# Performance work log

Measured on AMD Instinct MI355X. Metric: run time of the kernel, lower is better.

## Reference

```python
import jax, jax.numpy as jnp
import numpy as np

NUM_CLASSES = 1000
NUM_NEIGHBOURS = 200
SIGMA = 10.0
GAUSS_CONST = 1.0 / (2.0 * SIGMA ** 2)


def setup_inputs() -> dict:
    key = jax.random.key(0)
    k1, k2, k3 = jax.random.split(key, 3)
    B, D, C = 512, 512, 100000
    features = jax.random.normal(k1, (B, D), dtype=jnp.float32)
    centres = jax.random.normal(k2, (C, D), dtype=jnp.float32)
    centre_labels = jax.random.randint(k3, (C,), 0, NUM_CLASSES)
    weight = jnp.zeros((C,), dtype=jnp.float32)
    return {"features": features, "centres": centres,
            "centre_labels": centre_labels, "weight": weight}


def _knn(features, centres, k):
    # squared euclidean distances [B, C] without materializing [B, C, D]
    f2 = jnp.sum(features * features, axis=1, keepdims=True)      # [B,1]
    c2 = jnp.sum(centres * centres, axis=1)                        # [C]
    d2 = f2 + c2[None, :] - 2.0 * features @ centres.T             # [B,C]
    _, idx = jax.lax.top_k(-d2, k)                                 # smallest k
    return idx                                                     # [B,k]


def reference(features, centres, centre_labels, weight):
    B = features.shape[0]
    K = NUM_NEIGHBOURS
    nbr = _knn(features, centres, K)                               # [B,K] int
    gathered = centres[nbr]                                        # [B,K,D]
    d2 = jnp.sum((features[:, None, :] - gathered) ** 2, axis=-1)  # [B,K]
    kernel_weights = jnp.exp(weight)                               # [C]
    d = jnp.exp(-d2 * GAUSS_CONST) * kernel_weights[nbr]           # [B,K]
    nbr_labels = centre_labels[nbr]                                # [B,K]
    rows = jnp.arange(B)[:, None]
    p = jnp.zeros((B, NUM_CLASSES), dtype=d.dtype).at[rows, nbr_labels].add(d)
    p = jnp.where(p == 0, 1e-10, p)
    p = p / jnp.sum(p, axis=1, keepdims=True)
    return jnp.log(p)
```

## Files before the change

### kernel.cpp

```cpp
#include <hip/hip_runtime.h>
#include <hip/hip_fp16.h>
#include <math.h>
#include <stdint.h>

#define D_DIM    512
#define NCLS     1000
#define KSEL     200
#define NBINS    1024
#define HREP     4
#define CAND_MAX 2048
#define GCONST   0.005
#define MARGIN   4.0f

typedef short s8v __attribute__((ext_vector_type(8)));
typedef float f4v __attribute__((ext_vector_type(4)));

#define GLOAD_LDS16(gp, lp) __builtin_amdgcn_global_load_lds( \
    (const __attribute__((address_space(1))) void*)(gp),      \
    (__attribute__((address_space(3))) void*)(lp), 16, 0, 0)

static __device__ __forceinline__ unsigned short f2bf(float x) {
    unsigned u = __float_as_uint(x);
    return (unsigned short)((u + 0x7FFFu + ((u >> 16) & 1u)) >> 16);
}

static __device__ __forceinline__ unsigned cvt_pk_bf16(float lo, float hi) {
    unsigned r;
    asm("v_cvt_pk_bf16_f32 %0, %1, %2" : "=v"(r) : "v"(lo), "v"(hi));
    return r;
}

__global__ __launch_bounds__(256)
void convertF(const float* __restrict__ F, unsigned short* __restrict__ Fb,
              float* __restrict__ f2)
{
    __shared__ float red[256];
    const int r = blockIdx.x, t = threadIdx.x;
    float2 v = *(const float2*)(F + (size_t)r * D_DIM + t * 2);
    ushort2 o; o.x = f2bf(v.x); o.y = f2bf(v.y);
    *(ushort2*)(Fb + (size_t)r * D_DIM + t * 2) = o;
    red[t] = v.x * v.x + v.y * v.y;
    __syncthreads();
    for (int off = 128; off > 0; off >>= 1) {
        if (t < off) red[t] += red[t + off];
        __syncthreads();
    }
    if (t == 0) f2[r] = red[0];
}

__global__ __launch_bounds__(512)
void mfma_gemm(const unsigned short* __restrict__ Fb,
               const float* __restrict__ C,
               const float* __restrict__ f2,
               __half* __restrict__ Dm, int N)
{
    __shared__ short smem[2 * 256 * 64 + 128 * 64];
    short* BsBase = smem + 2 * 256 * 64;
    const int t    = threadIdx.x;
    const int lane = t & 63;
    const int w    = t >> 6;
    const int wm   = w >> 1, wn = w & 1;
    const int m0   = blockIdx.x * 256;
    const int n0   = blockIdx.y * 128;
    const int lrow = lane >> 3;
    const int oct  = (lane & 7) ^ lrow;
    const int quad = lane >> 4;
    const int col  = lane & 15;

    f4v acc[4][4];
#pragma unroll
    for (int i = 0; i < 4; ++i)
#pragma unroll
        for (int j = 0; j < 4; ++j) acc[i][j] = (f4v){0.f, 0.f, 0.f, 0.f};

    float  c2part[2] = {0.f, 0.f};
    float4 ra[2], rb[2];

#pragma unroll
    for (int cc = 0; cc < 2; ++cc) {
        int row = (w * 2 + cc) * 8 + lrow;
        int rg  = n0 + row; rg = rg < N ? rg : N - 1;
        const float* gp = C + (size_t)rg * D_DIM + oct * 8;
        ra[cc] = *(const float4*)gp;
        rb[cc] = *(const float4*)(gp + 4);
    }
#pragma unroll
    for (int cc = 0; cc < 4; ++cc) {
        int ch = w * 4 + cc;
        GLOAD_LDS16(Fb + (size_t)(m0 + ch * 8 + lrow) * D_DIM + 0 + oct * 8,
                    &smem[ch * 512]);
    }

    int buf = 0;
    for (int k0 = 0; k0 < D_DIM; k0 += 64, buf ^= 1) {
        short* As  = smem + buf * (256 * 64);
        short* Asn = smem + (buf ^ 1) * (256 * 64);
        short* Bs  = BsBase;

#pragma unroll
        for (int cc = 0; cc < 2; ++cc) {
            int row = (w * 2 + cc) * 8 + lrow;
            float4 va = ra[cc], vb = rb[cc];
            c2part[cc] += va.x*va.x + va.y*va.y + va.z*va.z + va.w*va.w
                        + vb.x*vb.x + vb.y*vb.y + vb.z*vb.z + vb.w*vb.w;
            uint4 o;
            o.x = cvt_pk_bf16(va.x, va.y);
            o.y = cvt_pk_bf16(va.z, va.w);
            o.z = cvt_pk_bf16(vb.x, vb.y);
            o.w = cvt_pk_bf16(vb.z, vb.w);
            *(uint4*)&Bs[row * 64 + (lane & 7) * 8] = o;
        }

        if (k0 + 64 < D_DIM) {
#pragma unroll
            for (int cc = 0; cc < 2; ++cc) {
                int row = (w * 2 + cc) * 8 + lrow;
                int rg  = n0 + row; rg = rg < N ? rg : N - 1;
                const float* gp = C + (size_t)rg * D_DIM + (k0 + 64) + oct * 8;
                ra[cc] = *(const float4*)gp;
                rb[cc] = *(const float4*)(gp + 4);
            }
#pragma unroll
            for (int cc = 0; cc < 4; ++cc) {
                int ch = w * 4 + cc;
                GLOAD_LDS16(Fb + (size_t)(m0 + ch * 8 + lrow) * D_DIM
                                + (k0 + 64) + oct * 8,
                            &Asn[ch * 512]);
            }
            asm volatile("s_waitcnt vmcnt(8) lgkmcnt(0)" ::: "memory");
        } else {
            asm volatile("s_waitcnt vmcnt(0) lgkmcnt(0)" ::: "memory");
        }
        __builtin_amdgcn_s_barrier();
        asm volatile("" ::: "memory");

#pragma unroll
        for (int kk = 0; kk < 2; ++kk) {
            int slot = (kk * 4 + quad) ^ (col & 7);
            s8v b[4];
#pragma unroll
            for (int j = 0; j < 4; ++j) {
                int row = wn * 64 + j * 16 + col;
                b[j] = *(s8v*)&Bs[row * 64 + slot * 8];
            }
            s8v a[4];
#pragma unroll
            for (int i = 0; i < 4; ++i) {
                int row = wm * 64 + i * 16 + col;
                a[i] = *(s8v*)&As[row * 64 + slot * 8];
            }
#pragma unroll
            for (int i = 0; i < 4; ++i)
#pragma unroll
                for (int j = 0; j < 4; ++j)
                    acc[i][j] = __builtin_amdgcn_mfma_f32_16x16x32_bf16(
                        a[i], b[j], acc[i][j], 0, 0, 0);
        }
        __builtin_amdgcn_s_barrier();
        asm volatile("" ::: "memory");
    }

    float* c2s = (float*)BsBase;
#pragma unroll
    for (int cc = 0; cc < 2; ++cc) {
        float s = c2part[cc];
        s += __shfl_xor(s, 1, 64);
        s += __shfl_xor(s, 2, 64);
        s += __shfl_xor(s, 4, 64);
        int row = (w * 2 + cc) * 8 + lrow;
        if ((lane & 7) == 0) c2s[row] = s;
    }
    __syncthreads();

    float c2v[4];
#pragma unroll
    for (int j = 0; j < 4; ++j)
        c2v[j] = c2s[wn * 64 + j * 16 + col];
    float fv[4][4];
#pragma unroll
    for (int i = 0; i < 4; ++i)
#pragma unroll
        for (int v = 0; v < 4; ++v)
            fv[i][v] = f2[m0 + wm * 64 + i * 16 + quad * 4 + v];

    __half* Cs = (__half*)smem;
#pragma unroll
    for (int h = 0; h < 2; ++h) {
        __syncthreads();
        if ((wm >> 1) == h) {
            int mlb = (wm & 1) * 64;
#pragma unroll
            for (int i = 0; i < 4; ++i) {
#pragma unroll
                for (int j = 0; j < 4; ++j) {
#pragma unroll
                    for (int v = 0; v < 4; ++v) {
                        int ml = mlb + i * 16 + quad * 4 + v;
                        int nl = wn * 64 + j * 16 + col;
                        float d2 = fv[i][v] + c2v[j] - 2.f * acc[i][j][v];
                        int slot = (nl >> 3) ^ (ml & 7);
                        Cs[ml * 128 + slot * 8 + (nl & 7)] = __float2half(d2);
                    }
                }
            }
        }
        __syncthreads();
#pragma unroll
        for (int it = 0; it < 4; ++it) {
            int idx = it * 512 + t;
            int row = idx >> 4;
            int o8  = idx & 15;
            int n   = n0 + o8 * 8;
            const __half* src = &Cs[row * 128 + ((o8 ^ (row & 7)) * 8)];
            __half* dst = Dm + (size_t)(m0 + h * 128 + row) * N + n;
            if (n + 7 < N) {
                *(uint4*)dst = *(const uint4*)src;
            } else if (n < N) {
                for (int e = 0; e < 8 && n + e < N; ++e) dst[e] = src[e];
            }
        }
    }
}

__global__ __launch_bounds__(1024)
void fused_select(const __half* __restrict__ Dm,
                  const float* __restrict__ F, const float* __restrict__ C,
                  const int* __restrict__ labels, const float* __restrict__ weight,
                  float* __restrict__ out, int N)
{
    __shared__ unsigned hist[NBINS * HREP];
    __shared__ float    fs[D_DIM];
    __shared__ int      idxs[CAND_MAX];
    __shared__ double   dists[CAND_MAX];
    __shared__ float    p[NCLS];
    __shared__ float    red[1024];
    __shared__ unsigned scanbuf[256];
    __shared__ float    sT;
    __shared__ unsigned scnt;

    const int r = blockIdx.x, t = threadIdx.x;
    for (int b = t; b < NBINS * HREP; b += 1024) hist[b] = 0u;
    for (int c = t; c < NCLS; c += 1024) p[c] = 0.f;
    for (int k = t; k < D_DIM; k += 1024) fs[k] = F[(size_t)r * D_DIM + k];
    if (t == 0) { sT = 1e30f; scnt = 0u; }
    __syncthreads();

    const __half* srow = Dm + (size_t)r * N;

    for (int j = t * 8; j < N; j += 8192) {
        uint4 sv = *(const uint4*)(srow + j);
        float2 s0 = __half22float2(*(__half2*)&sv.x);
        float2 s1 = __half22float2(*(__half2*)&sv.y);
        float2 s2 = __half22float2(*(__half2*)&sv.z);
        float2 s3 = __half22float2(*(__half2*)&sv.w);
        float d2v[8] = { s0.x, s0.y, s1.x, s1.y, s2.x, s2.y, s3.x, s3.y };
#pragma unroll
        for (int e = 0; e < 8; ++e) {
            int b = (int)(d2v[e] * 0.5f);
            b = b < 0 ? 0 : (b > NBINS - 1 ? NBINS - 1 : b);
            atomicAdd(&hist[(b << 2) + (t & 3)], 1u);
        }
    }
    __syncthreads();

    if (t < 256) {
        unsigned loc[NBINS / 256];
        unsigned s = 0;
#pragma unroll
        for (int i = 0; i < NBINS / 256; ++i) {
            int bb = t * (NBINS / 256) + i;
            loc[i] = hist[(bb << 2) + 0] + hist[(bb << 2) + 1]
                   + hist[(bb << 2) + 2] + hist[(bb << 2) + 3];
            s += loc[i];
        }
        scanbuf[t] = s;
        __syncthreads();
        unsigned pre = 0;
        for (int u = 0; u < t; ++u) pre += scanbuf[u];
        if (pre < KSEL && pre + s >= KSEL) {
            unsigned cum = pre;
            int b = NBINS - 1;
#pragma unroll
            for (int i = 0; i < NBINS / 256; ++i) {
                cum += loc[i];
                if (cum >= KSEL) { b = t * (NBINS / 256) + i; break; }
            }
            sT = 2.0f * (float)(b + 1) + MARGIN;
        }
    } else {
        __syncthreads();
    }
    __syncthreads();
    const float Tr = sT;

    for (int j = t * 8; j < N; j += 8192) {
        uint4 sv = *(const uint4*)(srow + j);
        float2 s0 = __half22float2(*(__half2*)&sv.x);
        float2 s1 = __half22float2(*(__half2*)&sv.y);
        float2 s2 = __half22float2(*(__half2*)&sv.z);
        float2 s3 = __half22float2(*(__half2*)&sv.w);
        float d2v[8] = { s0.x, s0.y, s1.x, s1.y, s2.x, s2.y, s3.x, s3.y };
#pragma unroll
        for (int e = 0; e < 8; ++e) {
            if (d2v[e] <= Tr) {
                unsigned pos = atomicAdd(&scnt, 1u);
                if (pos < CAND_MAX) idxs[pos] = j + e;
            }
        }
    }
    __syncthreads();
    int Nc = (int)scnt;
    if (Nc > CAND_MAX) Nc = CAND_MAX;

    {
        const int wv = t >> 6, lane = t & 63;
        for (int i = wv; i < Nc; i += 16) {
            int ci = idxs[i];
            const float* cp = C + (size_t)ci * D_DIM;
            float4 a  = *(const float4*)(cp + lane * 8);
            float4 b  = *(const float4*)(cp + lane * 8 + 4);
            float4 fa = *(const float4*)(fs + lane * 8);
            float4 fb = *(const float4*)(fs + lane * 8 + 4);
            double d0 = (double)fa.x - (double)a.x;
            double d1 = (double)fa.y - (double)a.y;
            double d2 = (double)fa.z - (double)a.z;
            double d3 = (double)fa.w - (double)a.w;
            double d4 = (double)fb.x - (double)b.x;
            double d5 = (double)fb.y - (double)b.y;
            double d6 = (double)fb.z - (double)b.z;
            double d7 = (double)fb.w - (double)b.w;
            double acc = d0*d0 + d1*d1 + d2*d2 + d3*d3
                       + d4*d4 + d5*d5 + d6*d6 + d7*d7;
#pragma unroll
            for (int off = 32; off > 0; off >>= 1)
                acc += __shfl_down(acc, off, 64);
            if (lane == 0) dists[i] = acc;
        }
    }
    __syncthreads();

    int ksel = KSEL < Nc ? KSEL : Nc;
    for (int i = t; i < Nc; i += 1024) {
        double di = dists[i];
        int    ii = idxs[i];
        int rank = 0;
        for (int j = 0; j < Nc; ++j) {
            double dj = dists[j];
            rank += (dj < di) || (dj == di && idxs[j] < ii);
        }
        if (rank < ksel) {
            double wgt = exp(-di * GCONST) * exp((double)weight[ii]);
            atomicAdd(&p[labels[ii]], (float)wgt);
        }
    }
    __syncthreads();

    float s = 0.f;
    for (int c = t; c < NCLS; c += 1024) {
        float v = p[c];
        if (v == 0.f) v = 1e-10f;
        p[c] = v;
        s += v;
    }
    red[t] = s;
    __syncthreads();
    for (int o = 512; o > 0; o >>= 1) {
        if (t < o) red[t] += red[t + o];
        __syncthreads();
    }
    float total = red[0];
    for (int c = t; c < NCLS; c += 1024)
        out[(size_t)r * NCLS + c] = logf(p[c] / total);
}

extern "C" void kernel_launch(void* const* d_in, const int* in_sizes, int n_in,
                              void* d_out, int out_size, void* d_ws, size_t ws_size,
                              hipStream_t stream)
{
    const float* features = (const float*)d_in[0];
    const float* centres  = (const float*)d_in[1];
    const int*   labels   = (const int*)d_in[2];
    const float* weight   = (const float*)d_in[3];
    const int B = in_sizes[0] / D_DIM;
    const int N = in_sizes[2];
    float* out = (float*)d_out;

    uint8_t* w = (uint8_t*)d_ws;
    size_t off = 0;
    auto alloc = [&](size_t bytes) -> uint8_t* {
        uint8_t* ptr = w + off;
        off = (off + bytes + 255) & ~(size_t)255;
        return ptr;
    };
    float*          f2 = (float*)alloc((size_t)B * 4);
    unsigned short* Fb = (unsigned short*)alloc((size_t)B * D_DIM * 2);
    __half*         Dm = (__half*)alloc((size_t)B * N * 2);
    (void)ws_size;

    convertF<<<B, 256, 0, stream>>>(features, Fb, f2);

    dim3 ggrid(B / 256, (N + 127) / 128);
    mfma_gemm<<<ggrid, 512, 0, stream>>>(Fb, centres, f2, Dm, N);

    fused_select<<<B, 1024, 0, stream>>>(Dm, features, centres,
                                         labels, weight, out, N);
}
```

Baseline: 444.3 us.

## Cover all 512 feature rows per GEMM block to read centres once

The GEMM block grows from 256x128 to 512x128 with 1024 threads, so each block spans every feature row and the grid runs only over centre tiles. Each fp32 centre row is now loaded and converted to bf16 once rather than by two separate M-blocks, which halves the dominant global read of the 200 MB centres matrix and removes duplicated c2 norm work. In exchange, LDS use grows to roughly 144 KB per block and there are half as many blocks, which may limit occupancy. The epilogue writes four 128-row halves and the load wait count is adjusted for the smaller number of per-thread centre loads.

```diff
diff --git a/kernel.cpp b/kernel.cpp
--- a/kernel.cpp
+++ b/kernel.cpp
@@ -48,20 +48,19 @@
     if (t == 0) f2[r] = red[0];
 }
 
-__global__ __launch_bounds__(512)
+__global__ __launch_bounds__(1024)
 void mfma_gemm(const unsigned short* __restrict__ Fb,
                const float* __restrict__ C,
                const float* __restrict__ f2,
                __half* __restrict__ Dm, int N)
 {
-    __shared__ short smem[2 * 256 * 64 + 128 * 64];
-    short* BsBase = smem + 2 * 256 * 64;
+    __shared__ short smem[2 * 512 * 64 + 128 * 64];
+    short* BsBase = smem + 2 * 512 * 64;
     const int t    = threadIdx.x;
     const int lane = t & 63;
     const int w    = t >> 6;
     const int wm   = w >> 1, wn = w & 1;
-    const int m0   = blockIdx.x * 256;
-    const int n0   = blockIdx.y * 128;
+    const int n0   = blockIdx.x * 128;
     const int lrow = lane >> 3;
     const int oct  = (lane & 7) ^ lrow;
     const int quad = lane >> 4;
@@ -73,61 +72,50 @@
 #pragma unroll
         for (int j = 0; j < 4; ++j) acc[i][j] = (f4v){0.f, 0.f, 0.f, 0.f};
 
-    float  c2part[2] = {0.f, 0.f};
-    float4 ra[2], rb[2];
-
-#pragma unroll
-    for (int cc = 0; cc < 2; ++cc) {
-        int row = (w * 2 + cc) * 8 + lrow;
-        int rg  = n0 + row; rg = rg < N ? rg : N - 1;
-        const float* gp = C + (size_t)rg * D_DIM + oct * 8;
-        ra[cc] = *(const float4*)gp;
-        rb[cc] = *(const float4*)(gp + 4);
-    }
+    float  c2part = 0.f;
+    float4 ra, rb;
+    const int brow = w * 8 + lrow;
+    int brg = n0 + brow; brg = brg < N ? brg : N - 1;
+    const float* Crow = C + (size_t)brg * D_DIM + oct * 8;
+
+    ra = *(const float4*)Crow;
+    rb = *(const float4*)(Crow + 4);
 #pragma unroll
     for (int cc = 0; cc < 4; ++cc) {
         int ch = w * 4 + cc;
-        GLOAD_LDS16(Fb + (size_t)(m0 + ch * 8 + lrow) * D_DIM + 0 + oct * 8,
+        GLOAD_LDS16(Fb + (size_t)(ch * 8 + lrow) * D_DIM + 0 + oct * 8,
                     &smem[ch * 512]);
     }
 
     int buf = 0;
     for (int k0 = 0; k0 < D_DIM; k0 += 64, buf ^= 1) {
-        short* As  = smem + buf * (256 * 64);
-        short* Asn = smem + (buf ^ 1) * (256 * 64);
+        short* As  = smem + buf * (512 * 64);
+        short* Asn = smem + (buf ^ 1) * (512 * 64);
         short* Bs  = BsBase;
 
-#pragma unroll
-        for (int cc = 0; cc < 2; ++cc) {
-            int row = (w * 2 + cc) * 8 + lrow;
-            float4 va = ra[cc], vb = rb[cc];
-            c2part[cc] += va.x*va.x + va.y*va.y + va.z*va.z + va.w*va.w
-                        + vb.x*vb.x + vb.y*vb.y + vb.z*vb.z + vb.w*vb.w;
+        {
+            float4 va = ra, vb = rb;
+            c2part += va.x*va.x + va.y*va.y + va.z*va.z + va.w*va.w
+                    + vb.x*vb.x + vb.y*vb.y + vb.z*vb.z + vb.w*vb.w;
             uint4 o;
             o.x = cvt_pk_bf16(va.x, va.y);
             o.y = cvt_pk_bf16(va.z, va.w);
             o.z = cvt_pk_bf16(vb.x, vb.y);
             o.w = cvt_pk_bf16(vb.z, vb.w);
-            *(uint4*)&Bs[row * 64 + (lane & 7) * 8] = o;
+            *(uint4*)&Bs[brow * 64 + (lane & 7) * 8] = o;
         }
 
         if (k0 + 64 < D_DIM) {
-#pragma unroll
-            for (int cc = 0; cc < 2; ++cc) {
-                int row = (w * 2 + cc) * 8 + lrow;
-                int rg  = n0 + row; rg = rg < N ? rg : N - 1;
-                const float* gp = C + (size_t)rg * D_DIM + (k0 + 64) + oct * 8;
-                ra[cc] = *(const float4*)gp;
-                rb[cc] = *(const float4*)(gp + 4);
-            }
+            ra = *(const float4*)(Crow + (k0 + 64));
+            rb = *(const float4*)(Crow + (k0 + 64) + 4);
 #pragma unroll
             for (int cc = 0; cc < 4; ++cc) {
                 int ch = w * 4 + cc;
-                GLOAD_LDS16(Fb + (size_t)(m0 + ch * 8 + lrow) * D_DIM
+                GLOAD_LDS16(Fb + (size_t)(ch * 8 + lrow) * D_DIM
                                 + (k0 + 64) + oct * 8,
                             &Asn[ch * 512]);
             }
-            asm volatile("s_waitcnt vmcnt(8) lgkmcnt(0)" ::: "memory");
+            asm volatile("s_waitcnt vmcnt(6) lgkmcnt(0)" ::: "memory");
         } else {
             asm volatile("s_waitcnt vmcnt(0) lgkmcnt(0)" ::: "memory");
         }
@@ -161,14 +149,12 @@
     }
 
     float* c2s = (float*)BsBase;
-#pragma unroll
-    for (int cc = 0; cc < 2; ++cc) {
-        float s = c2part[cc];
+    {
+        float s = c2part;
         s += __shfl_xor(s, 1, 64);
         s += __shfl_xor(s, 2, 64);
         s += __shfl_xor(s, 4, 64);
-        int row = (w * 2 + cc) * 8 + lrow;
-        if ((lane & 7) == 0) c2s[row] = s;
+        if ((lane & 7) == 0) c2s[brow] = s;
     }
     __syncthreads();
 
@@ -181,11 +167,11 @@
     for (int i = 0; i < 4; ++i)
 #pragma unroll
         for (int v = 0; v < 4; ++v)
-            fv[i][v] = f2[m0 + wm * 64 + i * 16 + quad * 4 + v];
+            fv[i][v] = f2[wm * 64 + i * 16 + quad * 4 + v];
 
     __half* Cs = (__half*)smem;
 #pragma unroll
-    for (int h = 0; h < 2; ++h) {
+    for (int h = 0; h < 4; ++h) {
         __syncthreads();
         if ((wm >> 1) == h) {
             int mlb = (wm & 1) * 64;
@@ -206,13 +192,13 @@
         }
         __syncthreads();
 #pragma unroll
-        for (int it = 0; it < 4; ++it) {
-            int idx = it * 512 + t;
+        for (int it = 0; it < 2; ++it) {
+            int idx = it * 1024 + t;
             int row = idx >> 4;
             int o8  = idx & 15;
             int n   = n0 + o8 * 8;
             const __half* src = &Cs[row * 128 + ((o8 ^ (row & 7)) * 8)];
-            __half* dst = Dm + (size_t)(m0 + h * 128 + row) * N + n;
+            __half* dst = Dm + (size_t)(h * 128 + row) * N + n;
             if (n + 7 < N) {
                 *(uint4*)dst = *(const uint4*)src;
             } else if (n < N) {
@@ -399,8 +385,7 @@
 
     convertF<<<B, 256, 0, stream>>>(features, Fb, f2);
 
-    dim3 ggrid(B / 256, (N + 127) / 128);
-    mfma_gemm<<<ggrid, 512, 0, stream>>>(Fb, centres, f2, Dm, N);
+    mfma_gemm<<<(N + 127) / 128, 1024, 0, stream>>>(Fb, centres, f2, Dm, N);
 
     fused_select<<<B, 1024, 0, stream>>>(Dm, features, centres,
                                          labels, weight, out, N);
```

New measurement: 619.3 us. 39.4% more time.
